# Kernel optimization log

Hardware: AMD Instinct MI355X
Metric: run time of the kernel (lower is better)

The kernel has to match this reference:

```python
import jax, jax.numpy as jnp
import numpy as np
from jax import lax

F = 88  # piano-roll feature dim, hard-coded in the original module


def setup_inputs() -> dict:
    key = jax.random.key(0)
    k1, k2, k3 = jax.random.split(key, 3)
    N, T, window = 128, 2048, 64
    x = jax.random.normal(k1, (N, T, F), dtype=jnp.float32)
    W = jax.random.normal(k2, (F, window * F), dtype=jnp.float32) * 0.02
    b = jax.random.normal(k3, (F,), dtype=jnp.float32) * 0.02
    return {"x": x, "W": W, "b": b}


def reference(x, W, b):
    # x: (N, T, F). Original: for each t, flatten x[:, t-window:t] (time-major),
    # LEFT-zero-pad to window*F, apply Linear(W, b). Exclusive of frame t, so the
    # effective receptive field for output t is frames [t-window, t-1] -> a
    # strictly-causal conv over time with kernel size `window`.
    N, T, _ = x.shape
    window = W.shape[1] // F
    # Left-pad `window` zero frames; window for output t is xp[:, t:t+window],
    # which equals x[:, t-window:t] with zeros filling missing early frames
    # (matching the original's left-side zero concat after flattening).
    xp = jnp.pad(x, ((0, 0), (window, 0), (0, 0)))  # (N, T+window, F)
    # Flattened index layout is tau*F + f, so W reshapes to (out=F, tau, f).
    K = W.reshape(F, window, F).transpose(1, 2, 0)  # WIO: (window, F_in, F_out)
    out = lax.conv_general_dilated(
        xp, K, window_strides=(1,), padding="VALID",
        dimension_numbers=("NWC", "WIO", "NWC"),
    )  # (N, T+1, F); valid starts 0..T, we need starts 0..T-1
    out = out[:, :T] + b  # (N, T, F)
    return (out, out)
```

## Files before the change

kernel.cpp:

```cpp
#include <hip/hip_runtime.h>
#include <hip/hip_bf16.h>

#define NBATCH 128
#define TLEN   2048
#define FDIM   88
#define WIN    64
#define TT     256
#define FRAMES (TT + WIN)
#define LSTR   104

typedef __attribute__((ext_vector_type(8))) short short8;
typedef __attribute__((ext_vector_type(4))) short short4v;
typedef __attribute__((ext_vector_type(4))) float floatx4;

static __device__ __forceinline__ unsigned short f2bf(float f) {
    union { float f; unsigned int u; } a; a.f = f;
    unsigned int u = a.u;
    u += 0x7fffu + ((u >> 16) & 1u);
    return (unsigned short)(u >> 16);
}

__global__ void prep_w(const float* __restrict__ W, unsigned short* __restrict__ Wt) {
    int idx = blockIdx.x * blockDim.x + threadIdx.x;
    if (idx >= WIN * 3 * 6 * 512) return;
    int j    = idx & 7;
    int lane = (idx >> 3) & 63;
    int rest = idx >> 9;
    int nt   = rest % 6;
    int kkt  = rest / 6;
    int kk   = kkt % 3;
    int tau  = kkt / 3;
    int n = nt * 16 + (lane & 15);
    int k = kk * 32 + (lane >> 4) * 8 + j;
    float v = 0.f;
    if (n < FDIM && k < FDIM) v = W[n * (WIN * FDIM) + tau * FDIM + k];
    Wt[idx] = f2bf(v);
}

__global__ __launch_bounds__(256, 2) void conv_mfma(
    const float* __restrict__ x, const unsigned short* __restrict__ Wt,
    const float* __restrict__ bias, float* __restrict__ out)
{
    __shared__ unsigned short xs[FRAMES * LSTR];

    const int tb  = blockIdx.x;
    const int nb  = blockIdx.y;
    const int t0  = tb * TT;
    const int tid = threadIdx.x;

    const float* xn = x + (size_t)nb * TLEN * FDIM;
    for (int idx = tid; idx < FRAMES * 26; idx += 256) {
        int i = idx / 26;
        int c = idx % 26;
        int g = t0 - WIN + i;
        short4v v = (short4v){0, 0, 0, 0};
        if (c < 22 && g >= 0) {
            float4 f = *((const float4*)(xn + (size_t)g * FDIM) + c);
            v.x = (short)f2bf(f.x); v.y = (short)f2bf(f.y);
            v.z = (short)f2bf(f.z); v.w = (short)f2bf(f.w);
        }
        *(short4v*)&xs[i * LSTR + c * 4] = v;
    }
    __syncthreads();

    const int wave = tid >> 6;
    const int lane = tid & 63;
    const int m    = lane & 15;
    const int quad = lane >> 4;
    const int wrow = wave * 64;

    floatx4 acc[4][6] = {};

    const int a_base = (wrow + m) * LSTR + quad * 8;
    const unsigned short* wt_lane = Wt + (size_t)lane * 8;

    for (int tau = 0; tau < WIN; ++tau) {
        const unsigned short* wt_tau = wt_lane + (size_t)tau * (18 * 512);
        const int a_tau = a_base + tau * LSTR;
        #pragma unroll
        for (int kk = 0; kk < 3; ++kk) {
            short8 bf[6];
            #pragma unroll
            for (int n_t = 0; n_t < 6; ++n_t)
                bf[n_t] = *(const short8*)(wt_tau + (kk * 6 + n_t) * 512);
            short8 af[4];
            #pragma unroll
            for (int m_t = 0; m_t < 4; ++m_t)
                af[m_t] = *(const short8*)&xs[a_tau + m_t * 16 * LSTR + kk * 32];
            __builtin_amdgcn_s_setprio(1);
            #pragma unroll
            for (int m_t = 0; m_t < 4; ++m_t)
                #pragma unroll
                for (int n_t = 0; n_t < 6; ++n_t)
                    acc[m_t][n_t] = __builtin_amdgcn_mfma_f32_16x16x32_bf16(
                        af[m_t], bf[n_t], acc[m_t][n_t], 0, 0, 0);
            __builtin_amdgcn_s_setprio(0);
        }
    }

    float bv[6];
    #pragma unroll
    for (int n_t = 0; n_t < 6; ++n_t) {
        int c = n_t * 16 + m;
        bv[n_t] = (c < FDIM) ? bias[c] : 0.f;
    }
    const size_t half = (size_t)NBATCH * TLEN * FDIM;
    #pragma unroll
    for (int n_t = 0; n_t < 6; ++n_t) {
        int c = n_t * 16 + m;
        if (c >= FDIM) continue;
        #pragma unroll
        for (int m_t = 0; m_t < 4; ++m_t) {
            #pragma unroll
            for (int reg = 0; reg < 4; ++reg) {
                int tr = wrow + m_t * 16 + quad * 4 + reg;
                size_t off = ((size_t)nb * TLEN + (t0 + tr)) * FDIM + c;
                float v = acc[m_t][n_t][reg] + bv[n_t];
                out[off] = v;
                out[half + off] = v;
            }
        }
    }
}

extern "C" void kernel_launch(void* const* d_in, const int* in_sizes, int n_in,
                              void* d_out, int out_size, void* d_ws, size_t ws_size,
                              hipStream_t stream) {
    const float* x = (const float*)d_in[0];
    const float* W = (const float*)d_in[1];
    const float* b = (const float*)d_in[2];
    float* out = (float*)d_out;
    unsigned short* Wt = (unsigned short*)d_ws;

    prep_w<<<(WIN * 3 * 6 * 512 + 255) / 256, 256, 0, stream>>>(W, Wt);
    dim3 grid(TLEN / TT, NBATCH);
    conv_mfma<<<grid, 256, 0, stream>>>(x, Wt, b, out);
}
```

Before: 518.5 us.

## Stage weight slices in LDS with double-buffered async loads and 2x2 wave split

Each time-tap weight slice is now prefetched into a double-buffered LDS area with global_load_lds, with a block barrier per tap, instead of every wave reading weights from global memory. The time tile is halved to 128 and the four waves are arranged 2x2 over rows and output columns, so each wave holds half the accumulators. The LDS row stride shrinks to 100. This is meant to cut repeated global/L2 weight traffic and register pressure. In exchange it adds a barrier per tap and halves x-tile reuse per block. The new stride also leaves 16-byte LDS reads only 8-byte aligned.

```diff
diff --git a/kernel.cpp b/kernel.cpp
--- a/kernel.cpp
+++ b/kernel.cpp
@@ -5,9 +5,11 @@
 #define TLEN   2048
 #define FDIM   88
 #define WIN    64
-#define TT     256
+#define TT     128
 #define FRAMES (TT + WIN)
-#define LSTR   104
+#define LSTR   100
+#define BSLICE (18 * 512)
+#define BCHUNK 1152
 
 typedef __attribute__((ext_vector_type(8))) short short8;
 typedef __attribute__((ext_vector_type(4))) short short4v;
@@ -20,9 +22,15 @@
     return (unsigned short)(u >> 16);
 }
 
+static __device__ __forceinline__ void gload_lds16(const unsigned short* g, unsigned short* l) {
+    __builtin_amdgcn_global_load_lds(
+        (const __attribute__((address_space(1))) unsigned int*)g,
+        (__attribute__((address_space(3))) unsigned int*)l, 16, 0, 0);
+}
+
 __global__ void prep_w(const float* __restrict__ W, unsigned short* __restrict__ Wt) {
     int idx = blockIdx.x * blockDim.x + threadIdx.x;
-    if (idx >= WIN * 3 * 6 * 512) return;
+    if (idx >= WIN * BSLICE) return;
     int j    = idx & 7;
     int lane = (idx >> 3) & 63;
     int rest = idx >> 9;
@@ -42,16 +50,20 @@
     const float* __restrict__ bias, float* __restrict__ out)
 {
     __shared__ unsigned short xs[FRAMES * LSTR];
+    __shared__ unsigned short bufB[2][BSLICE];
 
     const int tb  = blockIdx.x;
     const int nb  = blockIdx.y;
     const int t0  = tb * TT;
     const int tid = threadIdx.x;
 
+    for (int c = tid; c < BCHUNK; c += 256)
+        gload_lds16(Wt + (size_t)c * 8, &bufB[0][c * 8]);
+
     const float* xn = x + (size_t)nb * TLEN * FDIM;
-    for (int idx = tid; idx < FRAMES * 26; idx += 256) {
-        int i = idx / 26;
-        int c = idx % 26;
+    for (int idx = tid; idx < FRAMES * 25; idx += 256) {
+        int i = idx / 25;
+        int c = idx % 25;
         int g = t0 - WIN + i;
         short4v v = (short4v){0, 0, 0, 0};
         if (c < 22 && g >= 0) {
@@ -67,22 +79,29 @@
     const int lane = tid & 63;
     const int m    = lane & 15;
     const int quad = lane >> 4;
-    const int wrow = wave * 64;
+    const int wrow = (wave >> 1) * 64;
+    const int wcol = (wave & 1) * 48;
+    const int nt0  = (wave & 1) * 3;
 
-    floatx4 acc[4][6] = {};
+    floatx4 acc[4][3] = {};
 
     const int a_base = (wrow + m) * LSTR + quad * 8;
-    const unsigned short* wt_lane = Wt + (size_t)lane * 8;
 
     for (int tau = 0; tau < WIN; ++tau) {
-        const unsigned short* wt_tau = wt_lane + (size_t)tau * (18 * 512);
+        if (tau + 1 < WIN) {
+            const unsigned short* src = Wt + (size_t)(tau + 1) * BSLICE;
+            unsigned short* dst = bufB[(tau + 1) & 1];
+            for (int c = tid; c < BCHUNK; c += 256)
+                gload_lds16(src + c * 8, dst + c * 8);
+        }
+        const unsigned short* bp = bufB[tau & 1];
         const int a_tau = a_base + tau * LSTR;
         #pragma unroll
         for (int kk = 0; kk < 3; ++kk) {
-            short8 bf[6];
+            short8 bf[3];
             #pragma unroll
-            for (int n_t = 0; n_t < 6; ++n_t)
-                bf[n_t] = *(const short8*)(wt_tau + (kk * 6 + n_t) * 512);
+            for (int n_t = 0; n_t < 3; ++n_t)
+                bf[n_t] = *(const short8*)(bp + (kk * 6 + nt0 + n_t) * 512 + lane * 8);
             short8 af[4];
             #pragma unroll
             for (int m_t = 0; m_t < 4; ++m_t)
@@ -91,23 +110,24 @@
             #pragma unroll
             for (int m_t = 0; m_t < 4; ++m_t)
                 #pragma unroll
-                for (int n_t = 0; n_t < 6; ++n_t)
+                for (int n_t = 0; n_t < 3; ++n_t)
                     acc[m_t][n_t] = __builtin_amdgcn_mfma_f32_16x16x32_bf16(
                         af[m_t], bf[n_t], acc[m_t][n_t], 0, 0, 0);
             __builtin_amdgcn_s_setprio(0);
         }
+        __syncthreads();
     }
 
-    float bv[6];
+    float bv[3];
     #pragma unroll
-    for (int n_t = 0; n_t < 6; ++n_t) {
-        int c = n_t * 16 + m;
+    for (int n_t = 0; n_t < 3; ++n_t) {
+        int c = wcol + n_t * 16 + m;
         bv[n_t] = (c < FDIM) ? bias[c] : 0.f;
     }
     const size_t half = (size_t)NBATCH * TLEN * FDIM;
     #pragma unroll
-    for (int n_t = 0; n_t < 6; ++n_t) {
-        int c = n_t * 16 + m;
+    for (int n_t = 0; n_t < 3; ++n_t) {
+        int c = wcol + n_t * 16 + m;
         if (c >= FDIM) continue;
         #pragma unroll
         for (int m_t = 0; m_t < 4; ++m_t) {
@@ -132,7 +152,7 @@
     float* out = (float*)d_out;
     unsigned short* Wt = (unsigned short*)d_ws;
 
-    prep_w<<<(WIN * 3 * 6 * 512 + 255) / 256, 256, 0, stream>>>(W, Wt);
+    prep_w<<<(WIN * BSLICE + 255) / 256, 256, 0, stream>>>(W, Wt);
     dim3 grid(TLEN / TT, NBATCH);
     conv_mfma<<<grid, 256, 0, stream>>>(x, Wt, b, out);
 }
```

Measured after the change: 563.5 us. +8.7%, slower.

## Prefetch next-tap weight fragments into registers and shrink LDS row stride

Applied to the files above, without the earlier changes.

Weight fragments for each tap are now loaded from global memory into three register buffers one step ahead of the MFMA work that uses them. The first tap's fragments are issued before the shared-memory staging of x, so global-load latency overlaps with LDS fill and with matrix math instead of stalling each k-slice. The LDS row stride drops from 104 to 100 halfwords to change the bank mapping of the A-fragment reads. The trade-off is 18 short8 registers of weight data held live at once, which raises register pressure. The new 200-byte row stride also leaves 16-byte LDS reads only 8-byte aligned.

```diff
diff --git a/kernel.cpp b/kernel.cpp
--- a/kernel.cpp
+++ b/kernel.cpp
@@ -7,7 +7,8 @@
 #define WIN    64
 #define TT     256
 #define FRAMES (TT + WIN)
-#define LSTR   104
+#define LSTR   100
+#define BSLICE (18 * 512)
 
 typedef __attribute__((ext_vector_type(8))) short short8;
 typedef __attribute__((ext_vector_type(4))) short short4v;
@@ -22,7 +23,7 @@
 
 __global__ void prep_w(const float* __restrict__ W, unsigned short* __restrict__ Wt) {
     int idx = blockIdx.x * blockDim.x + threadIdx.x;
-    if (idx >= WIN * 3 * 6 * 512) return;
+    if (idx >= WIN * BSLICE) return;
     int j    = idx & 7;
     int lane = (idx >> 3) & 63;
     int rest = idx >> 9;
@@ -37,6 +38,30 @@
     Wt[idx] = f2bf(v);
 }
 
+static __device__ __forceinline__ void load6(short8* dst, const unsigned short* __restrict__ Wt,
+                                             int tau, int kk, int lane) {
+    const unsigned short* p = Wt + (size_t)tau * BSLICE + (size_t)(kk * 6 * 512) + lane * 8;
+    #pragma unroll
+    for (int n_t = 0; n_t < 6; ++n_t)
+        dst[n_t] = *(const short8*)(p + n_t * 512);
+}
+
+static __device__ __forceinline__ void mfma_step(floatx4 acc[4][6], const short8* bf,
+                                                 const unsigned short* xs, int a_off) {
+    short8 af[4];
+    #pragma unroll
+    for (int m_t = 0; m_t < 4; ++m_t)
+        af[m_t] = *(const short8*)&xs[a_off + m_t * 16 * LSTR];
+    __builtin_amdgcn_s_setprio(1);
+    #pragma unroll
+    for (int m_t = 0; m_t < 4; ++m_t)
+        #pragma unroll
+        for (int n_t = 0; n_t < 6; ++n_t)
+            acc[m_t][n_t] = __builtin_amdgcn_mfma_f32_16x16x32_bf16(
+                af[m_t], bf[n_t], acc[m_t][n_t], 0, 0, 0);
+    __builtin_amdgcn_s_setprio(0);
+}
+
 __global__ __launch_bounds__(256, 2) void conv_mfma(
     const float* __restrict__ x, const unsigned short* __restrict__ Wt,
     const float* __restrict__ bias, float* __restrict__ out)
@@ -48,10 +73,21 @@
     const int t0  = tb * TT;
     const int tid = threadIdx.x;
 
+    const int wave = tid >> 6;
+    const int lane = tid & 63;
+    const int m    = lane & 15;
+    const int quad = lane >> 4;
+    const int wrow = wave * 64;
+
+    short8 b0[6], b1[6], b2[6];
+    load6(b0, Wt, 0, 0, lane);
+    load6(b1, Wt, 0, 1, lane);
+    load6(b2, Wt, 0, 2, lane);
+
     const float* xn = x + (size_t)nb * TLEN * FDIM;
-    for (int idx = tid; idx < FRAMES * 26; idx += 256) {
-        int i = idx / 26;
-        int c = idx % 26;
+    for (int idx = tid; idx < FRAMES * 25; idx += 256) {
+        int i = idx / 25;
+        int c = idx % 25;
         int g = t0 - WIN + i;
         short4v v = (short4v){0, 0, 0, 0};
         if (c < 22 && g >= 0) {
@@ -63,39 +99,20 @@
     }
     __syncthreads();
 
-    const int wave = tid >> 6;
-    const int lane = tid & 63;
-    const int m    = lane & 15;
-    const int quad = lane >> 4;
-    const int wrow = wave * 64;
+    floatx4 acc[4][6] = {};
+    const int a_base = (wrow + m) * LSTR + quad * 8;
 
-    floatx4 acc[4][6] = {};
-
-    const int a_base = (wrow + m) * LSTR + quad * 8;
-    const unsigned short* wt_lane = Wt + (size_t)lane * 8;
-
-    for (int tau = 0; tau < WIN; ++tau) {
-        const unsigned short* wt_tau = wt_lane + (size_t)tau * (18 * 512);
-        const int a_tau = a_base + tau * LSTR;
-        #pragma unroll
-        for (int kk = 0; kk < 3; ++kk) {
-            short8 bf[6];
-            #pragma unroll
-            for (int n_t = 0; n_t < 6; ++n_t)
-                bf[n_t] = *(const short8*)(wt_tau + (kk * 6 + n_t) * 512);
-            short8 af[4];
-            #pragma unroll
-            for (int m_t = 0; m_t < 4; ++m_t)
-                af[m_t] = *(const short8*)&xs[a_tau + m_t * 16 * LSTR + kk * 32];
-            __builtin_amdgcn_s_setprio(1);
-            #pragma unroll
-            for (int m_t = 0; m_t < 4; ++m_t)
-                #pragma unroll
-                for (int n_t = 0; n_t < 6; ++n_t)
-                    acc[m_t][n_t] = __builtin_amdgcn_mfma_f32_16x16x32_bf16(
-                        af[m_t], bf[n_t], acc[m_t][n_t], 0, 0, 0);
-            __builtin_amdgcn_s_setprio(0);
-        }
+    for (int tau = 0; tau < WIN - 1; ++tau) {
+        const int at = a_base + tau * LSTR;
+        mfma_step(acc, b0, xs, at);          load6(b0, Wt, tau + 1, 0, lane);
+        mfma_step(acc, b1, xs, at + 32);     load6(b1, Wt, tau + 1, 1, lane);
+        mfma_step(acc, b2, xs, at + 64);     load6(b2, Wt, tau + 1, 2, lane);
+    }
+    {
+        const int at = a_base + (WIN - 1) * LSTR;
+        mfma_step(acc, b0, xs, at);
+        mfma_step(acc, b1, xs, at + 32);
+        mfma_step(acc, b2, xs, at + 64);
     }
 
     float bv[6];
@@ -132,7 +149,7 @@
     float* out = (float*)d_out;
     unsigned short* Wt = (unsigned short*)d_ws;
 
-    prep_w<<<(WIN * 3 * 6 * 512 + 255) / 256, 256, 0, stream>>>(W, Wt);
+    prep_w<<<(WIN * BSLICE + 255) / 256, 256, 0, stream>>>(W, Wt);
     dim3 grid(TLEN / TT, NBATCH);
     conv_mfma<<<grid, 256, 0, stream>>>(x, Wt, b, out);
 }
```

New measurement: 662.9 us. +27.9%, slower.
